# Optimization experiments

Hardware: AMD Instinct MI355X
Metric: run time of the kernel (lower is better)

The kernel has to match this reference:

```python
import jax, jax.numpy as jnp
import numpy as np

N = 20000        # num nodes
E = 320000       # num edges (avg degree 16)
INPUT_DIM = 256
D = 512          # d_model
FF = 2048        # dim_feedforward
OUT = 128        # output_linear out features
HDIM = 8         # LiteMLA per-head dim
KS = 5           # LiteMLA scale kernel size (scales=(5,))


def _layernorm(x, g, b, eps=1e-5):
    m = x.mean(-1, keepdims=True)
    v = ((x - m) ** 2).mean(-1, keepdims=True)
    return (x - m) * jax.lax.rsqrt(v + eps) * g + b


def _pos_encoding():
    # sin/cos table, d_model even branch of PositionalEncoding
    pos = np.arange(N, dtype=np.float32)[:, None]
    div = np.exp(np.arange(0, D, 2, dtype=np.float32) * (-np.log(10000.0) / D))
    pe = np.zeros((N, D), np.float32)
    pe[:, 0::2] = np.sin(pos * div)
    pe[:, 1::2] = np.cos(pos * div)
    return jnp.asarray(pe)


def _lite_mla(h, W_qkv, conv_w, W_proj, b_proj):
    # ReLU linear attention with one extra conv scale (kernel 5), per EfficientViT LiteMLA
    n, d = h.shape
    qkv = h @ W_qkv                               # [N, 3D]
    xc = qkv.T[None]                              # [1, 3D, N]
    ms = jax.lax.conv_general_dilated(
        xc, conv_w, window_strides=(1,), padding='SAME',
        feature_group_count=3 * D)                # depthwise conv over node axis
    ms = ms[0].T                                  # [N, 3D]
    full = jnp.concatenate([qkv, ms], axis=1)     # [N, 6D]
    heads = full.shape[1] // (3 * HDIM)           # 2 * D / HDIM
    t = full.reshape(n, heads, 3, HDIM)
    q = jax.nn.relu(t[:, :, 0])
    k = jax.nn.relu(t[:, :, 1])
    v = t[:, :, 2]
    v1 = jnp.concatenate([v, jnp.ones_like(v[..., :1])], axis=-1)  # append denom row
    kv = jnp.einsum('nhd,nhe->hde', k, v1)        # [h, HDIM, HDIM+1]
    o = jnp.einsum('nhd,hde->nhe', q, kv)         # [N, h, HDIM+1]
    o = o[..., :HDIM] / (o[..., HDIM:] + 1e-15)
    o = o.reshape(n, heads * HDIM)                # [N, 2D]
    return o @ W_proj + b_proj


def _fwd(x, edge_attr, pe, W_in, b_in, W_qkv, conv_w, W_proj, b_proj,
         g1, beta1, W1, bf1, W2, bf2, g2, beta2, W_out, b_out,
         edge_index, num_nodes):
    n = num_nodes
    h = x @ W_in + b_in
    h = h + pe[:n]                                # positional encoding (dropout=eval)
    # add self loops with weight 1
    loop = jnp.arange(n)
    row = jnp.concatenate([edge_index[0], loop])
    col = jnp.concatenate([edge_index[1], loop])
    w = jnp.concatenate([edge_attr, jnp.ones((n,), edge_attr.dtype)])
    # symmetric normalization: D^-1/2 W D^-1/2
    deg = jax.ops.segment_sum(w, row, num_segments=n)
    dis = jnp.where(deg > 0, jax.lax.rsqrt(jnp.maximum(deg, 1e-12)), 0.0)
    nw = dis[row] * w * dis[col]
    # attention + FFN (post-norm residuals as written)
    src2 = _lite_mla(h, W_qkv, conv_w, W_proj, b_proj)
    src = h + _layernorm(src2, g1, beta1)
    ff = jax.nn.relu(src @ W1 + bf1) @ W2 + bf2
    src = src + _layernorm(ff, g2, beta2)
    # sparse adjacency matmul: out[i] = sum_{e: row=i} nw_e * src[col_e]
    agg = jax.ops.segment_sum(nw[:, None] * src[col], row, num_segments=n)
    return jax.nn.relu(agg) @ W_out + b_out      # [N, OUT]


def setup_inputs() -> dict:
    key = jax.random.key(0)
    ks = jax.random.split(key, 10)
    s = lambda i, *sh: jax.random.normal(ks[i], sh, jnp.float32) * 0.02
    f32 = jnp.float32
    return {
        'x': jax.random.normal(ks[0], (N, INPUT_DIM), f32),
        'edge_index': jax.random.randint(ks[1], (2, E), 0, N),
        'edge_attr': jax.random.uniform(ks[2], (E,), f32),
        'num_nodes': N,
        'pe': _pos_encoding(),
        'W_in': s(3, INPUT_DIM, D), 'b_in': jnp.zeros((D,), f32),
        'W_qkv': s(4, D, 3 * D),
        'conv_w': s(5, 3 * D, 1, KS),
        'W_proj': s(6, 2 * D, D), 'b_proj': jnp.zeros((D,), f32),
        'g1': jnp.ones((D,), f32), 'beta1': jnp.zeros((D,), f32),
        'W1': s(7, D, FF), 'bf1': jnp.zeros((FF,), f32),
        'W2': s(8, FF, D), 'bf2': jnp.zeros((D,), f32),
        'g2': jnp.ones((D,), f32), 'beta2': jnp.zeros((D,), f32),
        'W_out': s(9, D, OUT), 'b_out': jnp.zeros((OUT,), f32),
    }


def reference(x, edge_index, edge_attr, num_nodes, pe, W_in, b_in, W_qkv, conv_w,
              W_proj, b_proj, g1, beta1, W1, bf1, W2, bf2, g2, beta2, W_out, b_out):
    return _fwd(x, edge_attr, pe, W_in, b_in, W_qkv, conv_w, W_proj, b_proj,
                g1, beta1, W1, bf1, W2, bf2, g2, beta2, W_out, b_out,
                edge_index, num_nodes)
```

## Files before the change

### kernel.cpp

```cpp
#include <hip/hip_runtime.h>

#define N_NODES 20000
#define N_EDGES 320000
#define DIN     256
#define DMODEL  512
#define TD      1536
#define FFD     2048
#define DOUT    128

typedef _Float16 f16;
typedef f16 f16x8 __attribute__((ext_vector_type(8)));
typedef f16 f16x4 __attribute__((ext_vector_type(4)));
typedef f16 f16x2 __attribute__((ext_vector_type(2)));
typedef float f32x4 __attribute__((ext_vector_type(4)));

__device__ __forceinline__ void cstore(float* p, float v) { *p = v; }
__device__ __forceinline__ void cstore(f16* p, float v)   { *p = (f16)v; }

#if defined(__has_builtin)
#if __has_builtin(__builtin_amdgcn_global_load_lds)
#define USE_GLOAD_LDS 1
#endif
#endif

template<typename TC, int HAS_BIAS, int HAS_ADD, int DO_RELU>
__global__ __launch_bounds__(256)
void gemm_mfma(const f16* __restrict__ A, const f16* __restrict__ Bt,
               const float* __restrict__ bias, const float* __restrict__ addmat,
               TC* __restrict__ C, f16* __restrict__ Cbf,
               int M, int N, int K)
{
    __shared__ f16 As[2][128 * 32];
    __shared__ f16 Bs[2][128 * 32];
    const int tid  = threadIdx.x;
    const int lane = tid & 63;
    const int wid  = tid >> 6;
    const int wm = wid >> 1, wn = wid & 1;
    const int m0 = blockIdx.y * 128, n0 = blockIdx.x * 128;

    f32x4 acc[4][4];
    #pragma unroll
    for (int i = 0; i < 4; ++i)
        #pragma unroll
        for (int j = 0; j < 4; ++j)
            acc[i][j] = (f32x4)0.0f;

    const int r  = lane & 15;
    const int kg = lane >> 4;
    const int px = (kg ^ ((r >> 1) & 3)) << 3;

#ifdef USE_GLOAD_LDS
    const int seg0 = wid * 2, seg1 = wid * 2 + 1;
    const int row0 = seg0 * 16 + (lane >> 2);
    const int row1 = seg1 * 16 + (lane >> 2);
    const int kc0  = (lane & 3) ^ ((row0 >> 1) & 3);
    const int kc1  = (lane & 3) ^ ((row1 >> 1) & 3);
    const f16* a0 = A  + (size_t)(m0 + row0) * K + kc0 * 8;
    const f16* a1 = A  + (size_t)(m0 + row1) * K + kc1 * 8;
    const f16* b0 = Bt + (size_t)(n0 + row0) * K + kc0 * 8;
    const f16* b1 = Bt + (size_t)(n0 + row1) * K + kc1 * 8;

    auto stage = [&](int buf, int k0) {
        __builtin_amdgcn_global_load_lds(
            (const __attribute__((address_space(1))) void*)(a0 + k0),
            (__attribute__((address_space(3))) void*)&As[buf][seg0 * 512], 16, 0, 0);
        __builtin_amdgcn_global_load_lds(
            (const __attribute__((address_space(1))) void*)(a1 + k0),
            (__attribute__((address_space(3))) void*)&As[buf][seg1 * 512], 16, 0, 0);
        __builtin_amdgcn_global_load_lds(
            (const __attribute__((address_space(1))) void*)(b0 + k0),
            (__attribute__((address_space(3))) void*)&Bs[buf][seg0 * 512], 16, 0, 0);
        __builtin_amdgcn_global_load_lds(
            (const __attribute__((address_space(1))) void*)(b1 + k0),
            (__attribute__((address_space(3))) void*)&Bs[buf][seg1 * 512], 16, 0, 0);
    };

    const int NT = K >> 5;
    stage(0, 0);
    for (int kt = 0; kt < NT; ++kt) {
        const int cur = kt & 1;
        if (kt + 1 < NT) {
            stage(cur ^ 1, (kt + 1) << 5);
            asm volatile("s_waitcnt vmcnt(4)" ::: "memory");
        } else {
            asm volatile("s_waitcnt vmcnt(0)" ::: "memory");
        }
        __builtin_amdgcn_s_barrier();
        __builtin_amdgcn_sched_barrier(0);
        f16x8 af[4], bfr[4];
        #pragma unroll
        for (int m = 0; m < 4; ++m)
            af[m] = *(const f16x8*)(&As[cur][(wm * 64 + m * 16 + r) * 32 + px]);
        #pragma unroll
        for (int n = 0; n < 4; ++n)
            bfr[n] = *(const f16x8*)(&Bs[cur][(wn * 64 + n * 16 + r) * 32 + px]);
        #pragma unroll
        for (int m = 0; m < 4; ++m)
            #pragma unroll
            for (int n = 0; n < 4; ++n)
                acc[m][n] = __builtin_amdgcn_mfma_f32_16x16x32_f16(
                    af[m], bfr[n], acc[m][n], 0, 0, 0);
        __builtin_amdgcn_sched_barrier(0);
        __builtin_amdgcn_s_barrier();
    }
#else
    for (int k0 = 0; k0 < K; k0 += 32) {
        #pragma unroll
        for (int it = 0; it < 2; ++it) {
            const int c   = tid + it * 256;
            const int row = c >> 2, kc = c & 3;
            const int widx = row * 32 + ((kc ^ ((row >> 1) & 3)) << 3);
            f16x8 va = {0, 0, 0, 0, 0, 0, 0, 0};
            const int ga = m0 + row;
            if (ga < M) va = *(const f16x8*)(A + (size_t)ga * K + k0 + kc * 8);
            *(f16x8*)(&As[0][widx]) = va;
            const f16x8 vb = *(const f16x8*)(Bt + (size_t)(n0 + row) * K + k0 + kc * 8);
            *(f16x8*)(&Bs[0][widx]) = vb;
        }
        __syncthreads();
        f16x8 af[4], bfr[4];
        #pragma unroll
        for (int m = 0; m < 4; ++m)
            af[m] = *(const f16x8*)(&As[0][(wm * 64 + m * 16 + r) * 32 + px]);
        #pragma unroll
        for (int n = 0; n < 4; ++n)
            bfr[n] = *(const f16x8*)(&Bs[0][(wn * 64 + n * 16 + r) * 32 + px]);
        #pragma unroll
        for (int m = 0; m < 4; ++m)
            #pragma unroll
            for (int n = 0; n < 4; ++n)
                acc[m][n] = __builtin_amdgcn_mfma_f32_16x16x32_f16(
                    af[m], bfr[n], acc[m][n], 0, 0, 0);
        __syncthreads();
    }
#endif

    const int rq = lane >> 4;
    #pragma unroll
    for (int m = 0; m < 4; ++m) {
        #pragma unroll
        for (int rr = 0; rr < 4; ++rr) {
            const int row = m0 + wm * 64 + m * 16 + rq * 4 + rr;
            if (row >= M) continue;
            #pragma unroll
            for (int n = 0; n < 4; ++n) {
                const int col = n0 + wn * 64 + n * 16 + (lane & 15);
                float v = acc[m][n][rr];
                if (HAS_BIAS) v += bias[col];
                if (HAS_ADD)  v += addmat[(size_t)row * N + col];
                if (DO_RELU)  v = fmaxf(v, 0.f);
                cstore(&C[(size_t)row * N + col], v);
                if (Cbf) Cbf[(size_t)row * N + col] = (f16)v;
            }
        }
    }
}

__global__ void wt_kernel(const float* __restrict__ W, f16* __restrict__ Wt, int K, int N)
{
    __shared__ float t[32][33];
    const int k0 = blockIdx.x * 32, n0 = blockIdx.y * 32;
    const int tx = threadIdx.x & 31, ty = threadIdx.x >> 5;
    #pragma unroll
    for (int i = ty; i < 32; i += 8) {
        const int k = k0 + i;
        if (k < K && n0 + tx < N) t[i][tx] = W[(size_t)k * N + n0 + tx];
    }
    __syncthreads();
    #pragma unroll
    for (int i = ty; i < 32; i += 8) {
        const int n = n0 + i;
        if (n < N && k0 + tx < K) Wt[(size_t)n * K + k0 + tx] = (f16)t[tx][i];
    }
}

__global__ void f2h_kernel(const float* __restrict__ in, f16* __restrict__ out, int n)
{
    const int i = (blockIdx.x * 256 + threadIdx.x) * 4;
    if (i < n) {
        const float4 v = *(const float4*)(in + i);
        out[i + 0] = (f16)v.x; out[i + 1] = (f16)v.y;
        out[i + 2] = (f16)v.z; out[i + 3] = (f16)v.w;
    }
}

#define KV_CHUNK 32
#define KV_BLOCKS (N_NODES / KV_CHUNK)
__global__ __launch_bounds__(256, 2)
void kv_fused_kernel(const f16* __restrict__ qkv, const float* __restrict__ cw,
                     f16* __restrict__ q_all, float* __restrict__ kvg,
                     float* __restrict__ kv_part)
{
    __shared__ f16 rows[5][TD];
    const int tid = threadIdx.x;
    const int n0 = blockIdx.x * KV_CHUNK;
    const int h = tid >> 1, d0 = (tid & 1) * 4;

    float wk[4][5], wv[8][5], wq[8][5];
    if (h >= 64) {
        const int cb = (h - 64) * 24;
        #pragma unroll
        for (int dd = 0; dd < 4; ++dd)
            #pragma unroll
            for (int t = 0; t < 5; ++t)
                wk[dd][t] = cw[(cb + 8 + d0 + dd) * 5 + t];
        #pragma unroll
        for (int e = 0; e < 8; ++e)
            #pragma unroll
            for (int t = 0; t < 5; ++t)
                wv[e][t] = cw[(cb + 16 + e) * 5 + t];
    }
    if (tid >= 64 && tid < 128) {
        const int cb = (tid - 64) * 24;
        #pragma unroll
        for (int d = 0; d < 8; ++d)
            #pragma unroll
            for (int t = 0; t < 5; ++t)
                wq[d][t] = cw[(cb + d) * 5 + t];
    }

    for (int r = n0 - 2; r <= n0 + 2; ++r) {
        const int slot = ((r % 5) + 5) % 5;
        if (tid < 192) {
            f16x8 v = {0, 0, 0, 0, 0, 0, 0, 0};
            if (r >= 0 && r < N_NODES)
                v = *(const f16x8*)(qkv + (size_t)r * TD + tid * 8);
            *(f16x8*)(&rows[slot][tid * 8]) = v;
        }
    }
    __syncthreads();

    float acc[36] = {};

    for (int i = 0; i < KV_CHUNK; ++i) {
        const int n = n0 + i;

        f16x8 pre = {0, 0, 0, 0, 0, 0, 0, 0};
        const bool doPre = (i < KV_CHUNK - 1) && (tid < 192);
        if (doPre && (n + 3) < N_NODES)
            pre = *(const f16x8*)(qkv + (size_t)(n + 3) * TD + tid * 8);

        const f16* wr[5] = { rows[(((n - 2) % 5) + 5) % 5],
                             rows[(((n - 1) % 5) + 5) % 5],
                             rows[n % 5],
                             rows[(n + 1) % 5],
                             rows[(n + 2) % 5] };

        float kv4[4], vv[8];
        if (h < 64) {
            const int cb = h * 24;
            const f16x4 kd = *(const f16x4*)(wr[2] + cb + 8 + d0);
            const f16x8 vd = *(const f16x8*)(wr[2] + cb + 16);
            #pragma unroll
            for (int dd = 0; dd < 4; ++dd) kv4[dd] = fmaxf((float)kd[dd], 0.f);
            #pragma unroll
            for (int e = 0; e < 8; ++e) vv[e] = (float)vd[e];
        } else {
            const int cb = (h - 64) * 24;
            f16x4 ka[5]; f16x8 va[5];
            #pragma unroll
            for (int t = 0; t < 5; ++t) {
                ka[t] = *(const f16x4*)(wr[t] + cb + 8 + d0);
                va[t] = *(const f16x8*)(wr[t] + cb + 16);
            }
            #pragma unroll
            for (int dd = 0; dd < 4; ++dd) {
                float s = 0.f;
                #pragma unroll
                for (int t = 0; t < 5; ++t) s = fmaf(wk[dd][t], (float)ka[t][dd], s);
                kv4[dd] = fmaxf(s, 0.f);
            }
            #pragma unroll
            for (int e = 0; e < 8; ++e) {
                float s = 0.f;
                #pragma unroll
                for (int t = 0; t < 5; ++t) s = fmaf(wv[e][t], (float)va[t][e], s);
                vv[e] = s;
            }
        }
        #pragma unroll
        for (int dd = 0; dd < 4; ++dd) {
            #pragma unroll
            for (int e = 0; e < 8; ++e)
                acc[dd * 9 + e] = fmaf(kv4[dd], vv[e], acc[dd * 9 + e]);
            acc[dd * 9 + 8] += kv4[dd];
        }

        if (tid < 128) {
            f16x8 qv;
            if (tid < 64) {
                qv = *(const f16x8*)(wr[2] + tid * 24);
                #pragma unroll
                for (int d = 0; d < 8; ++d)
                    qv[d] = qv[d] > (f16)0 ? qv[d] : (f16)0;
            } else {
                const int cb = (tid - 64) * 24;
                f16x8 qa[5];
                #pragma unroll
                for (int t = 0; t < 5; ++t) qa[t] = *(const f16x8*)(wr[t] + cb);
                #pragma unroll
                for (int d = 0; d < 8; ++d) {
                    float s = 0.f;
                    #pragma unroll
                    for (int t = 0; t < 5; ++t) s = fmaf(wq[d][t], (float)qa[t][d], s);
                    qv[d] = (f16)fmaxf(s, 0.f);
                }
            }
            *(f16x8*)(q_all + (size_t)n * 1024 + tid * 8) = qv;
        }

        __syncthreads();
        if (doPre)
            *(f16x8*)(&rows[(n + 3) % 5][tid * 8]) = pre;
        __syncthreads();
    }

    if (kv_part) {
        float* dst = kv_part + (size_t)blockIdx.x * 9216 + tid * 36;
        #pragma unroll
        for (int i = 0; i < 36; ++i) dst[i] = acc[i];
    } else {
        #pragma unroll
        for (int dd = 0; dd < 4; ++dd)
            #pragma unroll
            for (int e = 0; e < 9; ++e)
                atomicAdd(&kvg[h * 72 + (d0 + dd) * 9 + e], acc[dd * 9 + e]);
    }
}

__global__ void kv_reduce_kernel(const float* __restrict__ kv_part,
                                 float* __restrict__ kvg)
{
    const int j = blockIdx.x * 256 + threadIdx.x;
    float s = 0.f;
    for (int b = 0; b < KV_BLOCKS; ++b)
        s += kv_part[(size_t)b * 9216 + j];
    kvg[j] = s;
}

__global__ __launch_bounds__(256)
void attn_o_kernel(const f16* __restrict__ q_all, const float* __restrict__ kvg,
                   f16* __restrict__ o)
{
    __shared__ float kvt[72][128];
    const int tid = threadIdx.x;
    for (int i = tid; i < 9216; i += 256) {
        const int hh = i & 127, j = i >> 7;
        kvt[j][hh] = kvg[hh * 72 + j];
    }
    __syncthreads();
    const int h = tid & 127, sub = tid >> 7;
    for (int nb = blockIdx.x; nb < N_NODES / 2; nb += gridDim.x) {
        const int n = nb * 2 + sub;
        const f16x8 qv8 = *(const f16x8*)(q_all + (size_t)n * 1024 + h * 8);
        float q[8];
        #pragma unroll
        for (int d = 0; d < 8; ++d) q[d] = (float)qv8[d];
        float num[8], den = 0.f;
        #pragma unroll
        for (int e = 0; e < 8; ++e) {
            float s = 0.f;
            #pragma unroll
            for (int d = 0; d < 8; ++d) s = fmaf(q[d], kvt[d * 9 + e][h], s);
            num[e] = s;
        }
        #pragma unroll
        for (int d = 0; d < 8; ++d) den = fmaf(q[d], kvt[d * 9 + 8][h], den);
        const float rinv = 1.f / (den + 1e-15f);
        f16x8 ov;
        #pragma unroll
        for (int e = 0; e < 8; ++e) ov[e] = (f16)(num[e] * rinv);
        *(f16x8*)(o + (size_t)n * 1024 + h * 8) = ov;
    }
}

__global__ void ln_res_kernel(const f16* __restrict__ y, const f16* __restrict__ resid,
                              const float* __restrict__ g, const float* __restrict__ b,
                              f16* __restrict__ out_h)
{
    const int row = blockIdx.x;
    const int tid = threadIdx.x;
    const f16* yr = y + (size_t)row * DMODEL;
    const float v0 = (float)yr[tid], v1 = (float)yr[tid + 256];
    __shared__ float red[4], red2[4];
    float s = v0 + v1;
    #pragma unroll
    for (int o = 32; o > 0; o >>= 1) s += __shfl_down(s, o);
    if ((tid & 63) == 0) red[tid >> 6] = s;
    __syncthreads();
    const float mean = (red[0] + red[1] + red[2] + red[3]) * (1.0f / DMODEL);
    const float d0 = v0 - mean, d1 = v1 - mean;
    float q = d0 * d0 + d1 * d1;
    #pragma unroll
    for (int o = 32; o > 0; o >>= 1) q += __shfl_down(q, o);
    if ((tid & 63) == 0) red2[tid >> 6] = q;
    __syncthreads();
    const float var = (red2[0] + red2[1] + red2[2] + red2[3]) * (1.0f / DMODEL);
    const float inv = rsqrtf(var + 1e-5f);
    const f16* rr = resid + (size_t)row * DMODEL;
    const float o0 = (float)rr[tid]       + d0 * inv * g[tid]       + b[tid];
    const float o1 = (float)rr[tid + 256] + d1 * inv * g[tid + 256] + b[tid + 256];
    f16* oh = out_h + (size_t)row * DMODEL;
    oh[tid] = (f16)o0;
    oh[tid + 256] = (f16)o1;
}

__global__ void deg_init_kernel(float* __restrict__ deg)
{
    const int i = blockIdx.x * 256 + threadIdx.x;
    if (i < N_NODES) deg[i] = 1.0f;
}

__global__ void deg_acc_kernel(const int* __restrict__ eirow, const float* __restrict__ ea,
                               float* __restrict__ deg)
{
    const int e = blockIdx.x * 256 + threadIdx.x;
    if (e < N_EDGES) atomicAdd(&deg[eirow[e]], ea[e]);
}

__global__ void dis_kernel(const float* __restrict__ deg, float* __restrict__ dis)
{
    const int i = blockIdx.x * 256 + threadIdx.x;
    if (i < N_NODES) dis[i] = rsqrtf(deg[i]);
}

__global__ void count_kernel(const int* __restrict__ eirow, int* __restrict__ cnt)
{
    const int e = blockIdx.x * 256 + threadIdx.x;
    if (e < N_EDGES) atomicAdd(&cnt[eirow[e]], 1);
}

__global__ void scan_kernel(const int* __restrict__ cnt, int* __restrict__ rowstart,
                            int* __restrict__ cursor)
{
    __shared__ int ls[1024];
    const int tid = threadIdx.x;
    const int base = tid * 20;
    int local[20];
    int s = 0;
    #pragma unroll
    for (int i = 0; i < 20; ++i) {
        const int idx = base + i;
        const int v = (idx < N_NODES) ? cnt[idx] : 0;
        local[i] = s;
        s += v;
    }
    ls[tid] = s;
    __syncthreads();
    for (int off = 1; off < 1024; off <<= 1) {
        const int v = (tid >= off) ? ls[tid - off] : 0;
        __syncthreads();
        ls[tid] += v;
        __syncthreads();
    }
    const int excl = (tid == 0) ? 0 : ls[tid - 1];
    #pragma unroll
    for (int i = 0; i < 20; ++i) {
        const int idx = base + i;
        if (idx < N_NODES) {
            const int st = excl + local[i];
            rowstart[idx] = st;
            cursor[idx] = st;
        }
    }
    if (tid == 1023) rowstart[N_NODES] = ls[1023];
}

__global__ void scatter_kernel(const int* __restrict__ eirow, int* __restrict__ cursor,
                               int* __restrict__ sorted)
{
    const int e = blockIdx.x * 256 + threadIdx.x;
    if (e < N_EDGES) {
        const int r = eirow[e];
        const int p = atomicAdd(&cursor[r], 1);
        sorted[p] = e;
    }
}

__global__ __launch_bounds__(256)
void agg_kernel(const f16* __restrict__ srcf_h, const int* __restrict__ eicol,
                const float* __restrict__ ea, const float* __restrict__ dis,
                const int* __restrict__ rowstart, const int* __restrict__ sorted,
                f16* __restrict__ agg)
{
    __shared__ int   cbuf[256];
    __shared__ float wbuf[256];
    __shared__ float part[4][512];
    const int i = blockIdx.x;
    const int tid = threadIdx.x;
    const int lane = tid & 63, wv = tid >> 6;
    const float di = dis[i];
    const int s = rowstart[i];
    const int deg = rowstart[i + 1] - s;

    float acc[8] = {};
    for (int base = 0; base < deg; base += 256) {
        const int m = min(256, deg - base);
        if (tid < m) {
            const int e = sorted[s + base + tid];
            const int c = eicol[e];
            cbuf[tid] = c;
            wbuf[tid] = di * ea[e] * dis[c];
        }
        __syncthreads();
        #pragma unroll 2
        for (int p = wv; p < m; p += 4) {
            const int c = cbuf[p];
            const float w = wbuf[p];
            const f16x8 v = *(const f16x8*)(srcf_h + (size_t)c * DMODEL + lane * 8);
            #pragma unroll
            for (int j = 0; j < 8; ++j) acc[j] = fmaf(w, (float)v[j], acc[j]);
        }
        __syncthreads();
    }
    #pragma unroll
    for (int j = 0; j < 8; ++j) part[wv][lane * 8 + j] = acc[j];
    __syncthreads();
    const float wself = di * di;
    const f16x2 vs = *(const f16x2*)(srcf_h + (size_t)i * DMODEL + tid * 2);
    float a0 = wself * (float)vs[0], a1 = wself * (float)vs[1];
    #pragma unroll
    for (int w = 0; w < 4; ++w) {
        a0 += part[w][tid * 2];
        a1 += part[w][tid * 2 + 1];
    }
    f16x2 o;
    o[0] = (f16)fmaxf(a0, 0.f);
    o[1] = (f16)fmaxf(a1, 0.f);
    *(f16x2*)(agg + (size_t)i * DMODEL + tid * 2) = o;
}

static constexpr size_t OFF_HH    = 0;
static constexpr size_t OFF_FF    = 20480000ull;
static constexpr size_t OFF_QKV   = 40960000ull;
static constexpr size_t OFF_SRC2  = 40960000ull;
static constexpr size_t OFF_FFH   = 61440000ull;
static constexpr size_t OFF_AGG   = 61440000ull;
static constexpr size_t OFF_XH    = 102400000ull;
static constexpr size_t OFF_ATTN  = 102400000ull;
static constexpr size_t WT_IN     = 143360000ull;
static constexpr size_t WT_QKV    = 143622144ull;
static constexpr size_t WT_PROJ   = 145195008ull;
static constexpr size_t WT_W1     = 146243584ull;
static constexpr size_t WT_W2     = 148340736ull;
static constexpr size_t WT_OUT    = 150437888ull;
static constexpr size_t OFF_KV    = 150568960ull;
static constexpr size_t OFF_DEG   = 150605824ull;
static constexpr size_t OFF_DIS   = 150685824ull;
static constexpr size_t OFF_RS    = 150765824ull;
static constexpr size_t OFF_CUR   = 150845888ull;
static constexpr size_t OFF_CNT   = 150925888ull;
static constexpr size_t OFF_SORT  = 151005888ull;
static constexpr size_t OFF_KVP   = 152285888ull;
static constexpr size_t WS_NEED_KVP = 175325888ull;

extern "C" void kernel_launch(void* const* d_in, const int* in_sizes, int n_in,
                              void* d_out, int out_size, void* d_ws, size_t ws_size,
                              hipStream_t stream)
{
    const float* x      = (const float*)d_in[0];
    const int*   ei     = (const int*)d_in[1];
    const float* ea     = (const float*)d_in[2];
    const float* pe     = (const float*)d_in[4];
    const float* W_in   = (const float*)d_in[5];
    const float* b_in   = (const float*)d_in[6];
    const float* W_qkv  = (const float*)d_in[7];
    const float* conv_w = (const float*)d_in[8];
    const float* W_proj = (const float*)d_in[9];
    const float* b_proj = (const float*)d_in[10];
    const float* g1     = (const float*)d_in[11];
    const float* beta1  = (const float*)d_in[12];
    const float* W1     = (const float*)d_in[13];
    const float* bf1    = (const float*)d_in[14];
    const float* W2     = (const float*)d_in[15];
    const float* bf2    = (const float*)d_in[16];
    const float* g2     = (const float*)d_in[17];
    const float* beta2  = (const float*)d_in[18];
    const float* W_out  = (const float*)d_in[19];
    const float* b_out  = (const float*)d_in[20];

    char* ws = (char*)d_ws;
    f16*   h_h    = (f16*)(ws + OFF_HH);
    f16*   ff     = (f16*)(ws + OFF_FF);
    f16*   qkv    = (f16*)(ws + OFF_QKV);
    f16*   src2   = (f16*)(ws + OFF_SRC2);
    f16*   ffh    = (f16*)(ws + OFF_FFH);
    f16*   agg    = (f16*)(ws + OFF_AGG);
    f16*   x_h    = (f16*)(ws + OFF_XH);
    f16*   q_all  = (f16*)(ws + OFF_ATTN);
    f16*   wt_in   = (f16*)(ws + WT_IN);
    f16*   wt_qkv  = (f16*)(ws + WT_QKV);
    f16*   wt_proj = (f16*)(ws + WT_PROJ);
    f16*   wt_w1   = (f16*)(ws + WT_W1);
    f16*   wt_w2   = (f16*)(ws + WT_W2);
    f16*   wt_out  = (f16*)(ws + WT_OUT);
    float* kvg    = (float*)(ws + OFF_KV);
    float* deg    = (float*)(ws + OFF_DEG);
    float* dis    = (float*)(ws + OFF_DIS);
    int*   rs     = (int*)(ws + OFF_RS);
    int*   cur    = (int*)(ws + OFF_CUR);
    int*   cnt    = (int*)(ws + OFF_CNT);
    int*   sorted = (int*)(ws + OFF_SORT);
    float* outp   = (float*)d_out;

    const bool twoStage = (ws_size >= WS_NEED_KVP);
    float* kv_part = twoStage ? (float*)(ws + OFF_KVP) : nullptr;

    const int* eirow = ei;
    const int* eicol = ei + N_EDGES;

    if (!twoStage)
        hipMemsetAsync(kvg, 0, 9216 * sizeof(float), stream);
    hipMemsetAsync(cnt, 0, N_NODES * sizeof(int), stream);

    wt_kernel<<<dim3(DIN / 32,   DMODEL / 32), 256, 0, stream>>>(W_in,   wt_in,   DIN,    DMODEL);
    wt_kernel<<<dim3(DMODEL / 32, TD / 32),    256, 0, stream>>>(W_qkv,  wt_qkv,  DMODEL, TD);
    wt_kernel<<<dim3(1024 / 32,  DMODEL / 32), 256, 0, stream>>>(W_proj, wt_proj, 1024,   DMODEL);
    wt_kernel<<<dim3(DMODEL / 32, FFD / 32),   256, 0, stream>>>(W1,     wt_w1,   DMODEL, FFD);
    wt_kernel<<<dim3(FFD / 32,   DMODEL / 32), 256, 0, stream>>>(W2,     wt_w2,   FFD,    DMODEL);
    wt_kernel<<<dim3(DMODEL / 32, DOUT / 32),  256, 0, stream>>>(W_out,  wt_out,  DMODEL, DOUT);
    f2h_kernel<<<(N_NODES * DIN) / 1024, 256, 0, stream>>>(x, x_h, N_NODES * DIN);

    const int GY = (N_NODES + 127) / 128;

    gemm_mfma<f16, 1, 1, 0><<<dim3(DMODEL / 128, GY), 256, 0, stream>>>(
        x_h, wt_in, b_in, pe, h_h, nullptr, N_NODES, DMODEL, DIN);
    gemm_mfma<f16, 0, 0, 0><<<dim3(TD / 128, GY), 256, 0, stream>>>(
        h_h, wt_qkv, nullptr, nullptr, qkv, nullptr, N_NODES, TD, DMODEL);
    kv_fused_kernel<<<KV_BLOCKS, 256, 0, stream>>>(qkv, conv_w, q_all, kvg, kv_part);
    if (twoStage)
        kv_reduce_kernel<<<36, 256, 0, stream>>>(kv_part, kvg);
    attn_o_kernel<<<2500, 256, 0, stream>>>(q_all, kvg, q_all);
    gemm_mfma<f16, 1, 0, 0><<<dim3(DMODEL / 128, GY), 256, 0, stream>>>(
        q_all, wt_proj, b_proj, nullptr, src2, nullptr, N_NODES, DMODEL, 1024);
    ln_res_kernel<<<N_NODES, 256, 0, stream>>>(src2, h_h, g1, beta1, src2);
    gemm_mfma<f16, 1, 0, 1><<<dim3(FFD / 128, GY), 256, 0, stream>>>(
        src2, wt_w1, bf1, nullptr, ffh, nullptr, N_NODES, FFD, DMODEL);
    gemm_mfma<f16, 1, 0, 0><<<dim3(DMODEL / 128, GY), 256, 0, stream>>>(
        ffh, wt_w2, bf2, nullptr, ff, nullptr, N_NODES, DMODEL, FFD);
    ln_res_kernel<<<N_NODES, 256, 0, stream>>>(ff, src2, g2, beta2, ff);
    deg_init_kernel<<<(N_NODES + 255) / 256, 256, 0, stream>>>(deg);
    deg_acc_kernel<<<(N_EDGES + 255) / 256, 256, 0, stream>>>(eirow, ea, deg);
    dis_kernel<<<(N_NODES + 255) / 256, 256, 0, stream>>>(deg, dis);
    count_kernel<<<(N_EDGES + 255) / 256, 256, 0, stream>>>(eirow, cnt);
    scan_kernel<<<1, 1024, 0, stream>>>(cnt, rs, cur);
    scatter_kernel<<<(N_EDGES + 255) / 256, 256, 0, stream>>>(eirow, cur, sorted);
    agg_kernel<<<N_NODES, 256, 0, stream>>>(ff, eicol, ea, dis, rs, sorted, agg);
    gemm_mfma<float, 1, 0, 0><<<dim3(DOUT / 128, GY), 256, 0, stream>>>(
        agg, wt_out, b_out, nullptr, outp, nullptr, N_NODES, DOUT, DMODEL);
}
```

Before: 684.0 us.

## Triple-buffer GEMM LDS loads and stage f16 epilogue through shared memory

The MFMA GEMM moves from double to triple buffering: it prefetches two K-tiles ahead and waits with a looser vmcnt, so more global loads stay in flight behind the math. For f16 outputs the epilogue now writes results to LDS and then stores 16-byte vectors per row, replacing scattered 2-byte stores. The unused Cbf output is removed. Shared memory per block rises to 48 KB, which may lower occupancy, and the epilogue adds a block barrier.

```diff
diff --git a/kernel.cpp b/kernel.cpp
--- a/kernel.cpp
+++ b/kernel.cpp
@@ -27,11 +27,9 @@
 __global__ __launch_bounds__(256)
 void gemm_mfma(const f16* __restrict__ A, const f16* __restrict__ Bt,
                const float* __restrict__ bias, const float* __restrict__ addmat,
-               TC* __restrict__ C, f16* __restrict__ Cbf,
-               int M, int N, int K)
-{
-    __shared__ f16 As[2][128 * 32];
-    __shared__ f16 Bs[2][128 * 32];
+               TC* __restrict__ C, int M, int N, int K)
+{
+    __shared__ f16 smem[24576];
     const int tid  = threadIdx.x;
     const int lane = tid & 63;
     const int wid  = tid >> 6;
@@ -61,39 +59,46 @@
     const f16* b1 = Bt + (size_t)(n0 + row1) * K + kc1 * 8;
 
     auto stage = [&](int buf, int k0) {
+        f16* as = smem + buf * 4096;
+        f16* bs = smem + 12288 + buf * 4096;
         __builtin_amdgcn_global_load_lds(
             (const __attribute__((address_space(1))) void*)(a0 + k0),
-            (__attribute__((address_space(3))) void*)&As[buf][seg0 * 512], 16, 0, 0);
+            (__attribute__((address_space(3))) void*)&as[seg0 * 512], 16, 0, 0);
         __builtin_amdgcn_global_load_lds(
             (const __attribute__((address_space(1))) void*)(a1 + k0),
-            (__attribute__((address_space(3))) void*)&As[buf][seg1 * 512], 16, 0, 0);
+            (__attribute__((address_space(3))) void*)&as[seg1 * 512], 16, 0, 0);
         __builtin_amdgcn_global_load_lds(
             (const __attribute__((address_space(1))) void*)(b0 + k0),
-            (__attribute__((address_space(3))) void*)&Bs[buf][seg0 * 512], 16, 0, 0);
+            (__attribute__((address_space(3))) void*)&bs[seg0 * 512], 16, 0, 0);
         __builtin_amdgcn_global_load_lds(
             (const __attribute__((address_space(1))) void*)(b1 + k0),
-            (__attribute__((address_space(3))) void*)&Bs[buf][seg1 * 512], 16, 0, 0);
+            (__attribute__((address_space(3))) void*)&bs[seg1 * 512], 16, 0, 0);
     };
 
     const int NT = K >> 5;
     stage(0, 0);
+    if (NT > 1) stage(1, 32);
     for (int kt = 0; kt < NT; ++kt) {
-        const int cur = kt & 1;
-        if (kt + 1 < NT) {
-            stage(cur ^ 1, (kt + 1) << 5);
+        const int cur = kt % 3;
+        if (kt + 2 < NT) {
+            stage((kt + 2) % 3, (kt + 2) << 5);
+            asm volatile("s_waitcnt vmcnt(8)" ::: "memory");
+        } else if (kt + 1 < NT) {
             asm volatile("s_waitcnt vmcnt(4)" ::: "memory");
         } else {
             asm volatile("s_waitcnt vmcnt(0)" ::: "memory");
         }
         __builtin_amdgcn_s_barrier();
         __builtin_amdgcn_sched_barrier(0);
+        const f16* as = smem + cur * 4096;
+        const f16* bs = smem + 12288 + cur * 4096;
         f16x8 af[4], bfr[4];
         #pragma unroll
         for (int m = 0; m < 4; ++m)
-            af[m] = *(const f16x8*)(&As[cur][(wm * 64 + m * 16 + r) * 32 + px]);
+            af[m] = *(const f16x8*)(&as[(wm * 64 + m * 16 + r) * 32 + px]);
         #pragma unroll
         for (int n = 0; n < 4; ++n)
-            bfr[n] = *(const f16x8*)(&Bs[cur][(wn * 64 + n * 16 + r) * 32 + px]);
+            bfr[n] = *(const f16x8*)(&bs[(wn * 64 + n * 16 + r) * 32 + px]);
         #pragma unroll
         for (int m = 0; m < 4; ++m)
             #pragma unroll
@@ -113,18 +118,18 @@
             f16x8 va = {0, 0, 0, 0, 0, 0, 0, 0};
             const int ga = m0 + row;
             if (ga < M) va = *(const f16x8*)(A + (size_t)ga * K + k0 + kc * 8);
-            *(f16x8*)(&As[0][widx]) = va;
+            *(f16x8*)(&smem[widx]) = va;
             const f16x8 vb = *(const f16x8*)(Bt + (size_t)(n0 + row) * K + k0 + kc * 8);
-            *(f16x8*)(&Bs[0][widx]) = vb;
+            *(f16x8*)(&smem[12288 + widx]) = vb;
         }
         __syncthreads();
         f16x8 af[4], bfr[4];
         #pragma unroll
         for (int m = 0; m < 4; ++m)
-            af[m] = *(const f16x8*)(&As[0][(wm * 64 + m * 16 + r) * 32 + px]);
+            af[m] = *(const f16x8*)(&smem[(wm * 64 + m * 16 + r) * 32 + px]);
         #pragma unroll
         for (int n = 0; n < 4; ++n)
-            bfr[n] = *(const f16x8*)(&Bs[0][(wn * 64 + n * 16 + r) * 32 + px]);
+            bfr[n] = *(const f16x8*)(&smem[12288 + (wn * 64 + n * 16 + r) * 32 + px]);
         #pragma unroll
         for (int m = 0; m < 4; ++m)
             #pragma unroll
@@ -136,21 +141,49 @@
 #endif
 
     const int rq = lane >> 4;
-    #pragma unroll
-    for (int m = 0; m < 4; ++m) {
-        #pragma unroll
-        for (int rr = 0; rr < 4; ++rr) {
-            const int row = m0 + wm * 64 + m * 16 + rq * 4 + rr;
-            if (row >= M) continue;
-            #pragma unroll
-            for (int n = 0; n < 4; ++n) {
-                const int col = n0 + wn * 64 + n * 16 + (lane & 15);
-                float v = acc[m][n][rr];
-                if (HAS_BIAS) v += bias[col];
-                if (HAS_ADD)  v += addmat[(size_t)row * N + col];
-                if (DO_RELU)  v = fmaxf(v, 0.f);
-                cstore(&C[(size_t)row * N + col], v);
-                if (Cbf) Cbf[(size_t)row * N + col] = (f16)v;
+    if constexpr (sizeof(TC) == 2) {
+        #pragma unroll
+        for (int m = 0; m < 4; ++m) {
+            #pragma unroll
+            for (int rr = 0; rr < 4; ++rr) {
+                const int rl = wm * 64 + m * 16 + rq * 4 + rr;
+                #pragma unroll
+                for (int n = 0; n < 4; ++n) {
+                    const int cl = wn * 64 + n * 16 + (lane & 15);
+                    float v = acc[m][n][rr];
+                    if (HAS_BIAS) v += bias[n0 + cl];
+                    if (HAS_ADD && (m0 + rl) < M) v += addmat[(size_t)(m0 + rl) * N + n0 + cl];
+                    if (DO_RELU) v = fmaxf(v, 0.f);
+                    smem[rl * 128 + cl] = (f16)v;
+                }
+            }
+        }
+        __syncthreads();
+        #pragma unroll
+        for (int i = 0; i < 8; ++i) {
+            const int ch  = tid + i * 256;
+            const int row = ch >> 4;
+            const int cc  = (ch & 15) << 3;
+            if (m0 + row < M)
+                *(f16x8*)((f16*)C + (size_t)(m0 + row) * N + n0 + cc) =
+                    *(const f16x8*)(&smem[row * 128 + cc]);
+        }
+    } else {
+        #pragma unroll
+        for (int m = 0; m < 4; ++m) {
+            #pragma unroll
+            for (int rr = 0; rr < 4; ++rr) {
+                const int row = m0 + wm * 64 + m * 16 + rq * 4 + rr;
+                if (row >= M) continue;
+                #pragma unroll
+                for (int n = 0; n < 4; ++n) {
+                    const int col = n0 + wn * 64 + n * 16 + (lane & 15);
+                    float v = acc[m][n][rr];
+                    if (HAS_BIAS) v += bias[col];
+                    if (HAS_ADD)  v += addmat[(size_t)row * N + col];
+                    if (DO_RELU)  v = fmaxf(v, 0.f);
+                    cstore(&C[(size_t)row * N + col], v);
+                }
             }
         }
     }
@@ -624,20 +657,20 @@
     const int GY = (N_NODES + 127) / 128;
 
     gemm_mfma<f16, 1, 1, 0><<<dim3(DMODEL / 128, GY), 256, 0, stream>>>(
-        x_h, wt_in, b_in, pe, h_h, nullptr, N_NODES, DMODEL, DIN);
+        x_h, wt_in, b_in, pe, h_h, N_NODES, DMODEL, DIN);
     gemm_mfma<f16, 0, 0, 0><<<dim3(TD / 128, GY), 256, 0, stream>>>(
-        h_h, wt_qkv, nullptr, nullptr, qkv, nullptr, N_NODES, TD, DMODEL);
+        h_h, wt_qkv, nullptr, nullptr, qkv, N_NODES, TD, DMODEL);
     kv_fused_kernel<<<KV_BLOCKS, 256, 0, stream>>>(qkv, conv_w, q_all, kvg, kv_part);
     if (twoStage)
         kv_reduce_kernel<<<36, 256, 0, stream>>>(kv_part, kvg);
     attn_o_kernel<<<2500, 256, 0, stream>>>(q_all, kvg, q_all);
     gemm_mfma<f16, 1, 0, 0><<<dim3(DMODEL / 128, GY), 256, 0, stream>>>(
-        q_all, wt_proj, b_proj, nullptr, src2, nullptr, N_NODES, DMODEL, 1024);
+        q_all, wt_proj, b_proj, nullptr, src2, N_NODES, DMODEL, 1024);
     ln_res_kernel<<<N_NODES, 256, 0, stream>>>(src2, h_h, g1, beta1, src2);
     gemm_mfma<f16, 1, 0, 1><<<dim3(FFD / 128, GY), 256, 0, stream>>>(
-        src2, wt_w1, bf1, nullptr, ffh, nullptr, N_NODES, FFD, DMODEL);
+        src2, wt_w1, bf1, nullptr, ffh, N_NODES, FFD, DMODEL);
     gemm_mfma<f16, 1, 0, 0><<<dim3(DMODEL / 128, GY), 256, 0, stream>>>(
-        ffh, wt_w2, bf2, nullptr, ff, nullptr, N_NODES, DMODEL, FFD);
+        ffh, wt_w2, bf2, nullptr, ff, N_NODES, DMODEL, FFD);
     ln_res_kernel<<<N_NODES, 256, 0, stream>>>(ff, src2, g2, beta2, ff);
     deg_init_kernel<<<(N_NODES + 255) / 256, 256, 0, stream>>>(deg);
     deg_acc_kernel<<<(N_EDGES + 255) / 256, 256, 0, stream>>>(eirow, ea, deg);
@@ -647,5 +680,5 @@
     scatter_kernel<<<(N_EDGES + 255) / 256, 256, 0, stream>>>(eirow, cur, sorted);
     agg_kernel<<<N_NODES, 256, 0, stream>>>(ff, eicol, ea, dis, rs, sorted, agg);
     gemm_mfma<float, 1, 0, 0><<<dim3(DOUT / 128, GY), 256, 0, stream>>>(
-        agg, wt_out, b_out, nullptr, outp, nullptr, N_NODES, DOUT, DMODEL);
-}
+        agg, wt_out, b_out, nullptr, outp, N_NODES, DOUT, DMODEL);
+}
```

New measurement: 622.0 us. 9.1% less time.
